# Kernel tuning notes

Hardware: AMD Instinct MI355X
Metric: run time of the kernel (lower is better)

The kernel has to match this reference:

```python
import jax, jax.numpy as jnp
import numpy as np

B, L, M = 4, 2048, 1024
G, E = 8, 8
CAP_FACTOR = 2.0

def _ffn_size(m, widening=8.0):
    f = int(widening * m) * 2 // 3
    return f + (8 - f) % 8

H = _ffn_size(M)  # 5464


def setup_inputs():
    key = jax.random.key(0)
    k0, k1, k2, k3, k4 = jax.random.split(key, 5)
    return {
        "inputs": jax.random.normal(k0, (B, L, M), jnp.float32),
        "router_w": jax.random.normal(k1, (M, E), jnp.float32) * 0.02,
        "w0_kernel": jax.random.normal(k2, (E, M, H), jnp.float32) * 0.02,
        "w1_kernel": jax.random.normal(k3, (E, M, H), jnp.float32) * 0.02,
        "wo_kernel": jax.random.normal(k4, (E, H, M), jnp.float32) * 0.02,
    }


def _gating_top2(logits, C):
    # logits: (G, S, E) -> dispatch, combine: (G, S, E, C)
    Gd, Sd, Ed = logits.shape
    raw = jax.nn.softmax(logits, axis=-1)
    idx1 = jnp.argmax(raw, axis=-1)
    m1 = jax.nn.one_hot(idx1, Ed, dtype=logits.dtype)
    gate1 = jnp.sum(raw * m1, axis=-1)
    rest = raw * (1.0 - m1)
    idx2 = jnp.argmax(rest, axis=-1)
    m2 = jax.nn.one_hot(idx2, Ed, dtype=logits.dtype)
    gate2 = jnp.sum(rest * m2, axis=-1)
    # exclusive cumsum along S gives position in expert queue
    p1 = jnp.cumsum(m1, axis=-2) - m1
    m1 = m1 * (p1 < C).astype(m1.dtype)
    p1 = jnp.sum(p1 * m1, axis=-1)
    m1_flat = jnp.sum(m1, axis=-1)
    m1_count = jnp.sum(m1, axis=-2)  # (G, E)
    p2 = jnp.cumsum(m2, axis=-2) - m2 + m1_count[:, None, :]
    m2 = m2 * (p2 < C).astype(m2.dtype)
    p2 = jnp.sum(p2 * m2, axis=-1)
    m2_flat = jnp.sum(m2, axis=-1)
    gate1 = gate1 * m1_flat
    gate2 = gate2 * m2_flat
    c1 = (gate1[..., None] * jax.nn.one_hot(idx1, Ed, dtype=jnp.float32))[..., None] \
         * jax.nn.one_hot(p1.astype(jnp.int32), C, dtype=jnp.float32)[:, :, None, :]
    c2 = (gate2[..., None] * jax.nn.one_hot(idx2, Ed, dtype=jnp.float32))[..., None] \
         * jax.nn.one_hot(p2.astype(jnp.int32), C, dtype=jnp.float32)[:, :, None, :]
    combine = (c1 + c2).astype(logits.dtype)
    dispatch = (combine != 0).astype(logits.dtype)
    return dispatch, combine


def reference(inputs, router_w, w0_kernel, w1_kernel, wo_kernel):
    Bb, Ll, Mm = inputs.shape
    S = Bb * Ll // G
    x = inputs.reshape(G, S, Mm)
    logits = jnp.einsum('GSM,ME->GSE', x, router_w)
    cap = int(CAP_FACTOR * S / E)
    C = (cap + 3) // 4 * 4
    dispatch, combine = _gating_top2(logits, C)
    expert_inputs = jnp.einsum('GSEC,GSM->EGCM', dispatch, x)
    layer_w0 = jnp.einsum('EGCM,EMH->EGCH', expert_inputs, w0_kernel)
    layer_w1 = jnp.einsum('EGCM,EMH->EGCH', expert_inputs, w1_kernel)
    hidden = jax.nn.gelu(layer_w0, approximate=True) * layer_w1
    expert_outputs = jnp.einsum('EGCH,EHM->EGCM', hidden, wo_kernel)
    out = jnp.einsum('EGCM,GSEC->GSM', expert_outputs, combine)
    return out.reshape(Bb, Ll, Mm)
```

## Files before the change

kernel.cpp:

```cpp
#include <hip/hip_runtime.h>
#include <cstdint>
#include <cstddef>

constexpr int G = 8;
constexpr int S = 1024;
constexpr int E = 8;
constexpr int MD = 1024;
constexpr int H = 5464;
constexpr int HP = 5504;
constexpr int CAP = 256;
constexpr int T = G * S;
constexpr int GC = G * CAP;

typedef __bf16 bf16;
typedef __bf16 bf16x8 __attribute__((ext_vector_type(8)));
typedef __bf16 bf16x4 __attribute__((ext_vector_type(4)));
typedef float f32x4 __attribute__((ext_vector_type(4)));

__device__ __forceinline__ void async16(const void* g, void* l) {
    __builtin_amdgcn_global_load_lds((__attribute__((address_space(1))) void*)(g),
                                     (__attribute__((address_space(3))) void*)(l),
                                     16, 0, 0);
}

__device__ __forceinline__ float gelu_tanh(float x) {
    return 0.5f * x * (1.0f + tanhf(0.7978845608028654f * (x + 0.044715f * x * x * x)));
}

__device__ __forceinline__ int sw_elem(int row, int gi) {
    return (row * 8 + (gi ^ (row & 7))) * 8;
}

__global__ void router_k(const float* __restrict__ x, const float* __restrict__ rw,
                         int* __restrict__ idx1, int* __restrict__ idx2,
                         float* __restrict__ gate1, float* __restrict__ gate2) {
    int wave = threadIdx.x >> 6, lane = threadIdx.x & 63;
    int t = blockIdx.x * 4 + wave;
    const float* xr = x + (size_t)t * MD;
    float acc[E];
#pragma unroll
    for (int e = 0; e < E; e++) acc[e] = 0.0f;
    for (int m = lane; m < MD; m += 64) {
        float xv = xr[m];
        const float* w = rw + m * E;
#pragma unroll
        for (int e = 0; e < E; e++) acc[e] += xv * w[e];
    }
#pragma unroll
    for (int off = 32; off > 0; off >>= 1) {
#pragma unroll
        for (int e = 0; e < E; e++) acc[e] += __shfl_xor(acc[e], off, 64);
    }
    if (lane == 0) {
        float mx = acc[0];
#pragma unroll
        for (int e = 1; e < E; e++) mx = fmaxf(mx, acc[e]);
        float raw[E]; float sum = 0.0f;
#pragma unroll
        for (int e = 0; e < E; e++) { raw[e] = expf(acc[e] - mx); sum += raw[e]; }
        float inv = 1.0f / sum;
#pragma unroll
        for (int e = 0; e < E; e++) raw[e] *= inv;
        int i1 = 0; float b1 = raw[0];
#pragma unroll
        for (int e = 1; e < E; e++) if (raw[e] > b1) { b1 = raw[e]; i1 = e; }
        int i2 = 0; float b2 = -1.0f;
#pragma unroll
        for (int e = 0; e < E; e++) {
            float v = (e == i1) ? 0.0f : raw[e];
            if (v > b2) { b2 = v; i2 = e; }
        }
        idx1[t] = i1; idx2[t] = i2; gate1[t] = b1; gate2[t] = b2;
    }
}

__global__ void scan_k(const int* __restrict__ idx1, const int* __restrict__ idx2,
                       const float* __restrict__ gate1, const float* __restrict__ gate2,
                       int* __restrict__ tok1, int* __restrict__ tok2,
                       float* __restrict__ g1m, float* __restrict__ g2m,
                       int* __restrict__ slot_src, int* __restrict__ fill) {
    int g = blockIdx.x;
    int lane = threadIdx.x;
    unsigned long long lt = (1ull << lane) - 1ull;
    int cnt1[E], cnt2[E];
#pragma unroll
    for (int e = 0; e < E; e++) { cnt1[e] = 0; cnt2[e] = 0; }
    for (int ch = 0; ch < S / 64; ch++) {
        int s = ch * 64 + lane, t = g * S + s;
        int i1 = idx1[t];
        int p = 0;
#pragma unroll
        for (int e = 0; e < E; e++) {
            unsigned long long m = __ballot(i1 == e);
            if (i1 == e) p = cnt1[e] + (int)__popcll(m & lt);
            cnt1[e] += (int)__popcll(m);
        }
        bool kept = p < CAP;
        tok1[t] = kept ? (i1 * CAP + p) : -1;
        g1m[t] = kept ? gate1[t] : 0.0f;
        if (kept) slot_src[((i1 * G + g) << 8) + p] = s;
    }
    int m1c[E];
#pragma unroll
    for (int e = 0; e < E; e++) m1c[e] = min(cnt1[e], CAP);
    for (int ch = 0; ch < S / 64; ch++) {
        int s = ch * 64 + lane, t = g * S + s;
        int i2 = idx2[t];
        float g2 = gate2[t];
        int p = 0;
#pragma unroll
        for (int e = 0; e < E; e++) {
            unsigned long long m = __ballot(i2 == e);
            if (i2 == e) p = m1c[e] + cnt2[e] + (int)__popcll(m & lt);
            cnt2[e] += (int)__popcll(m);
        }
        bool kept = p < CAP;
        bool nz = (g2 != 0.0f);
        tok2[t] = (kept && nz) ? (i2 * CAP + p) : -1;
        g2m[t] = (kept && nz) ? g2 : 0.0f;
        if (kept) slot_src[((i2 * G + g) << 8) + p] = nz ? s : -1;
    }
    if (lane < E) fill[lane * G + g] = min(m1c[lane] + cnt2[lane], CAP);
}

__global__ void gather_k(const float* __restrict__ x, const int* __restrict__ slot_src,
                         const int* __restrict__ fill, bf16* __restrict__ ein) {
    int slot = blockIdx.x;
    int c = slot & 255, g = (slot >> 8) & 7, e = slot >> 11;
    int i = threadIdx.x * 4;
    int src = (c < fill[e * G + g]) ? slot_src[slot] : -1;
    bf16x4 v;
    if (src >= 0) {
        float4 f = *(const float4*)(x + ((size_t)(g * S + src)) * MD + i);
        v[0] = (bf16)f.x; v[1] = (bf16)f.y; v[2] = (bf16)f.z; v[3] = (bf16)f.w;
    } else {
        v[0] = (bf16)0.0f; v[1] = (bf16)0.0f; v[2] = (bf16)0.0f; v[3] = (bf16)0.0f;
    }
    *(bf16x4*)(ein + (size_t)slot * MD + i) = v;
}

__global__ void transpose_cast_k(const float* __restrict__ in, bf16* __restrict__ out,
                                 int R, int Cc, int Rp, int Cp) {
    __shared__ float lds[64][65];
    int c0 = blockIdx.x * 64;
    int r0 = blockIdx.y * 64;
    const float* bin = in + (size_t)blockIdx.z * R * Cc;
    bf16* bout = out + (size_t)blockIdx.z * Cp * Rp;
    int tid = threadIdx.x;
    int lr = tid >> 4;
    int lc = (tid & 15) * 4;
#pragma unroll
    for (int i = 0; i < 4; i++) {
        int r = r0 + lr + i * 16;
        float v0 = 0, v1 = 0, v2 = 0, v3 = 0;
        if (r < R) {
            const float* p = bin + (size_t)r * Cc + c0 + lc;
            if (c0 + lc + 3 < Cc) {
                float4 f = *(const float4*)p;
                v0 = f.x; v1 = f.y; v2 = f.z; v3 = f.w;
            } else {
                if (c0 + lc + 0 < Cc) v0 = p[0];
                if (c0 + lc + 1 < Cc) v1 = p[1];
                if (c0 + lc + 2 < Cc) v2 = p[2];
                if (c0 + lc + 3 < Cc) v3 = p[3];
            }
        }
        lds[lr + i * 16][lc + 0] = v0;
        lds[lr + i * 16][lc + 1] = v1;
        lds[lr + i * 16][lc + 2] = v2;
        lds[lr + i * 16][lc + 3] = v3;
    }
    __syncthreads();
    int orr = tid >> 2;
    int oc = (tid & 3) * 16;
    bf16x8 o0, o1;
#pragma unroll
    for (int j = 0; j < 8; j++) o0[j] = (bf16)lds[oc + j][orr];
#pragma unroll
    for (int j = 0; j < 8; j++) o1[j] = (bf16)lds[oc + 8 + j][orr];
    bf16* dst = bout + (size_t)(c0 + orr) * Rp + r0 + oc;
    *(bf16x8*)(dst) = o0;
    *(bf16x8*)(dst + 8) = o1;
}

__global__ __launch_bounds__(256, 3) void gemm1_k(const bf16* __restrict__ ein,
                                                  const bf16* __restrict__ w0t,
                                                  const bf16* __restrict__ w1t,
                                                  bf16* __restrict__ hidden) {
    int rt = blockIdx.x, nt = blockIdx.y, e = blockIdx.z;
    __shared__ __align__(16) bf16 As[128 * 64];
    __shared__ __align__(16) bf16 B0s[64 * 64];
    __shared__ __align__(16) bf16 B1s[64 * 64];
    int lane = threadIdx.x & 63, wave = threadIdx.x >> 6;
    int wm = wave & 1, wn = wave >> 1;
    const bf16* A  = ein + ((size_t)e * GC + rt * 128) * MD;
    const bf16* B0 = w0t + ((size_t)e * HP + nt * 64) * MD;
    const bf16* B1 = w1t + ((size_t)e * HP + nt * 64) * MD;
    f32x4 acc0[4][2], acc1[4][2];
    f32x4 z = {0.0f, 0.0f, 0.0f, 0.0f};
#pragma unroll
    for (int i = 0; i < 4; i++)
#pragma unroll
        for (int j = 0; j < 2; j++) { acc0[i][j] = z; acc1[i][j] = z; }
    int lr = lane >> 3, ls = lane & 7;
#pragma unroll 1
    for (int kt = 0; kt < MD / 64; kt++) {
        __syncthreads();
        int k0 = kt * 64;
#pragma unroll
        for (int i = 0; i < 4; i++) {
            int c = i * 4 + wave;
            int r = c * 8 + lr;
            int gj = ls ^ (r & 7);
            async16(A + (size_t)r * MD + k0 + gj * 8, &As[c * 512]);
        }
#pragma unroll
        for (int i = 0; i < 2; i++) {
            int c = i * 4 + wave;
            int r = c * 8 + lr;
            int gj = ls ^ (r & 7);
            size_t go = (size_t)r * MD + k0 + gj * 8;
            async16(B0 + go, &B0s[c * 512]);
            async16(B1 + go, &B1s[c * 512]);
        }
        __syncthreads();
#pragma unroll
        for (int ks = 0; ks < 2; ks++) {
            bf16x8 af[4], b0f[2], b1f[2];
            int gi = ks * 4 + (lane >> 4);
            int mrow = wm * 64 + (lane & 15);
            int nrow = wn * 32 + (lane & 15);
#pragma unroll
            for (int i = 0; i < 4; i++) af[i] = *(const bf16x8*)&As[sw_elem(mrow + i * 16, gi)];
#pragma unroll
            for (int j = 0; j < 2; j++) {
                b0f[j] = *(const bf16x8*)&B0s[sw_elem(nrow + j * 16, gi)];
                b1f[j] = *(const bf16x8*)&B1s[sw_elem(nrow + j * 16, gi)];
            }
#pragma unroll
            for (int i = 0; i < 4; i++)
#pragma unroll
                for (int j = 0; j < 2; j++) {
                    acc0[i][j] = __builtin_amdgcn_mfma_f32_16x16x32_bf16(af[i], b0f[j], acc0[i][j], 0, 0, 0);
                    acc1[i][j] = __builtin_amdgcn_mfma_f32_16x16x32_bf16(af[i], b1f[j], acc1[i][j], 0, 0, 0);
                }
        }
    }
    bf16* Hb = hidden + (size_t)e * GC * HP;
    int colb = nt * 64 + wn * 32 + (lane & 15);
    int rowb = rt * 128 + wm * 64 + ((lane >> 4) * 4);
#pragma unroll
    for (int i = 0; i < 4; i++)
#pragma unroll
        for (int j = 0; j < 2; j++) {
            int col = colb + j * 16;
            bool ok = col < H;
#pragma unroll
            for (int r = 0; r < 4; r++) {
                int row = rowb + i * 16 + r;
                float v = ok ? gelu_tanh(acc0[i][j][r]) * acc1[i][j][r] : 0.0f;
                Hb[(size_t)row * HP + col] = (bf16)v;
            }
        }
}

__global__ __launch_bounds__(256) void gemm2_k(const bf16* __restrict__ hidden,
                                               const bf16* __restrict__ wot,
                                               float* __restrict__ eout) {
    int rt = blockIdx.x, nt = blockIdx.y, e = blockIdx.z;
    __shared__ __align__(16) bf16 As[128 * 64];
    __shared__ __align__(16) bf16 Bs[128 * 64];
    int lane = threadIdx.x & 63, wave = threadIdx.x >> 6;
    int wm = wave & 1, wn = wave >> 1;
    const bf16* A = hidden + ((size_t)e * GC + rt * 128) * HP;
    const bf16* B = wot + ((size_t)e * MD + nt * 128) * HP;
    f32x4 acc[4][4];
    f32x4 z = {0.0f, 0.0f, 0.0f, 0.0f};
#pragma unroll
    for (int i = 0; i < 4; i++)
#pragma unroll
        for (int j = 0; j < 4; j++) acc[i][j] = z;
    int lr = lane >> 3, ls = lane & 7;
#pragma unroll 1
    for (int kt = 0; kt < HP / 64; kt++) {
        __syncthreads();
        int k0 = kt * 64;
#pragma unroll
        for (int i = 0; i < 4; i++) {
            int R0 = (i * 4 + wave) * 8;
            int r = R0 + lr;
            int gj = ls ^ (r & 7);
            size_t go = (size_t)r * HP + k0 + gj * 8;
            async16(A + go, &As[R0 * 64]);
            async16(B + go, &Bs[R0 * 64]);
        }
        __syncthreads();
#pragma unroll
        for (int ks = 0; ks < 2; ks++) {
            bf16x8 af[4], bf[4];
            int gi = ks * 4 + (lane >> 4);
            int mrow = wm * 64 + (lane & 15);
            int nrow = wn * 64 + (lane & 15);
#pragma unroll
            for (int i = 0; i < 4; i++) {
                af[i] = *(const bf16x8*)&As[sw_elem(mrow + i * 16, gi)];
                bf[i] = *(const bf16x8*)&Bs[sw_elem(nrow + i * 16, gi)];
            }
#pragma unroll
            for (int i = 0; i < 4; i++)
#pragma unroll
                for (int j = 0; j < 4; j++)
                    acc[i][j] = __builtin_amdgcn_mfma_f32_16x16x32_bf16(af[i], bf[j], acc[i][j], 0, 0, 0);
        }
    }
    float* Ob = eout + (size_t)e * GC * MD;
    int colb = nt * 128 + wn * 64 + (lane & 15);
    int rowb = rt * 128 + wm * 64 + ((lane >> 4) * 4);
#pragma unroll
    for (int i = 0; i < 4; i++)
#pragma unroll
        for (int j = 0; j < 4; j++) {
            int col = colb + j * 16;
#pragma unroll
            for (int r = 0; r < 4; r++) {
                int row = rowb + i * 16 + r;
                Ob[(size_t)row * MD + col] = acc[i][j][r];
            }
        }
}

__global__ void combine_k(const float* __restrict__ eout, const int* __restrict__ tok1,
                          const int* __restrict__ tok2, const float* __restrict__ g1m,
                          const float* __restrict__ g2m, float* __restrict__ out) {
    int t = blockIdx.x;
    int g = t >> 10;
    int i = threadIdx.x * 4;
    int r1 = tok1[t], r2 = tok2[t];
    float f1 = g1m[t], f2 = g2m[t];
    float4 o = {0, 0, 0, 0};
    if (r1 >= 0) {
        size_t row = (size_t)(((r1 >> 8) * G + g) * CAP + (r1 & 255));
        float4 v = *(const float4*)(eout + row * MD + i);
        o.x += f1 * v.x; o.y += f1 * v.y; o.z += f1 * v.z; o.w += f1 * v.w;
    }
    if (r2 >= 0) {
        size_t row = (size_t)(((r2 >> 8) * G + g) * CAP + (r2 & 255));
        float4 v = *(const float4*)(eout + row * MD + i);
        o.x += f2 * v.x; o.y += f2 * v.y; o.z += f2 * v.z; o.w += f2 * v.w;
    }
    *(float4*)(out + (size_t)t * MD + i) = o;
}

constexpr size_t SZ_TI = (size_t)T * 4;
constexpr size_t OFF_IDX1 = 0;
constexpr size_t OFF_IDX2 = OFF_IDX1 + SZ_TI;
constexpr size_t OFF_GT1  = OFF_IDX2 + SZ_TI;
constexpr size_t OFF_GT2  = OFF_GT1 + SZ_TI;
constexpr size_t OFF_G1M  = OFF_GT2 + SZ_TI;
constexpr size_t OFF_G2M  = OFF_G1M + SZ_TI;
constexpr size_t OFF_TK1  = OFF_G2M + SZ_TI;
constexpr size_t OFF_TK2  = OFF_TK1 + SZ_TI;
constexpr size_t OFF_SLOT = OFF_TK2 + SZ_TI;
constexpr size_t OFF_FILL = OFF_SLOT + (size_t)E * G * CAP * 4;
constexpr size_t OFF_EIN  = (OFF_FILL + (size_t)E * G * 4 + 255) & ~(size_t)255;
constexpr size_t OFF_W0T  = OFF_EIN + (size_t)E * GC * MD * 2;
constexpr size_t OFF_W1T  = OFF_W0T + (size_t)E * HP * MD * 2;
constexpr size_t OFF_WOT  = OFF_W1T + (size_t)E * HP * MD * 2;
constexpr size_t OFF_HID  = OFF_WOT + (size_t)E * MD * HP * 2;
constexpr size_t OFF_EOUT = OFF_HID + (size_t)E * GC * HP * 2;

extern "C" void kernel_launch(void* const* d_in, const int* in_sizes, int n_in,
                              void* d_out, int out_size, void* d_ws, size_t ws_size,
                              hipStream_t stream) {
    const float* x  = (const float*)d_in[0];
    const float* rw = (const float*)d_in[1];
    const float* w0 = (const float*)d_in[2];
    const float* w1 = (const float*)d_in[3];
    const float* wo = (const float*)d_in[4];
    float* out = (float*)d_out;
    char* ws = (char*)d_ws;

    int*   idx1 = (int*)(ws + OFF_IDX1);
    int*   idx2 = (int*)(ws + OFF_IDX2);
    float* gt1  = (float*)(ws + OFF_GT1);
    float* gt2  = (float*)(ws + OFF_GT2);
    float* g1m  = (float*)(ws + OFF_G1M);
    float* g2m  = (float*)(ws + OFF_G2M);
    int*   tk1  = (int*)(ws + OFF_TK1);
    int*   tk2  = (int*)(ws + OFF_TK2);
    int*   slot = (int*)(ws + OFF_SLOT);
    int*   fill = (int*)(ws + OFF_FILL);
    bf16*  ein  = (bf16*)(ws + OFF_EIN);
    bf16*  w0t  = (bf16*)(ws + OFF_W0T);
    bf16*  w1t  = (bf16*)(ws + OFF_W1T);
    bf16*  wot  = (bf16*)(ws + OFF_WOT);
    bf16*  hid  = (bf16*)(ws + OFF_HID);
    float* eout = (float*)(ws + OFF_EOUT);

    router_k<<<T / 4, 256, 0, stream>>>(x, rw, idx1, idx2, gt1, gt2);
    scan_k<<<G, 64, 0, stream>>>(idx1, idx2, gt1, gt2, tk1, tk2, g1m, g2m, slot, fill);
    gather_k<<<E * G * CAP, 256, 0, stream>>>(x, slot, fill, ein);
    transpose_cast_k<<<dim3(HP / 64, MD / 64, E), 256, 0, stream>>>(w0, w0t, MD, H, MD, HP);
    transpose_cast_k<<<dim3(HP / 64, MD / 64, E), 256, 0, stream>>>(w1, w1t, MD, H, MD, HP);
    transpose_cast_k<<<dim3(MD / 64, HP / 64, E), 256, 0, stream>>>(wo, wot, H, MD, HP, MD);
    gemm1_k<<<dim3(GC / 128, HP / 64, E), 256, 0, stream>>>(ein, w0t, w1t, hid);
    gemm2_k<<<dim3(GC / 128, MD / 128, E), 256, 0, stream>>>(hid, wot, eout);
    combine_k<<<T, 256, 0, stream>>>(eout, tk1, tk2, g1m, g2m, out);
}
```

Before: 1.249 ms.

## Use 256x256 double-buffered 8-wave GEMM core with interleaved w0/w1 layout

Both expert GEMMs now share a 256x256 output tile core run by 512 threads. It double-buffers LDS, prefetches half-tiles between MFMA quadrants, raises wave priority during MFMA and uses explicit waitcnt/barrier control. The w0 and w1 transposes write into one interleaved buffer in 128-column blocks, so gemm1 runs as a single GEMM over width 2*HP. The GELU-times-w1 product is formed in the epilogue from paired accumulators, and block IDs are swizzled for L2 locality. This targets low arithmetic intensity and unhidden load latency, at the cost of 128KB of LDS per block and hand-written synchronization that is fragile.

After: 1.208 ms. 3.3% less time.

```diff
diff --git a/kernel.cpp b/kernel.cpp
--- a/kernel.cpp
+++ b/kernel.cpp
@@ -8,9 +8,11 @@
 constexpr int MD = 1024;
 constexpr int H = 5464;
 constexpr int HP = 5504;
+constexpr int N1 = 2 * HP;
 constexpr int CAP = 256;
 constexpr int T = G * S;
 constexpr int GC = G * CAP;
+constexpr int BK = 64;
 
 typedef __bf16 bf16;
 typedef __bf16 bf16x8 __attribute__((ext_vector_type(8)));
@@ -30,6 +32,11 @@
 __device__ __forceinline__ int sw_elem(int row, int gi) {
     return (row * 8 + (gi ^ (row & 7))) * 8;
 }
+
+#define BARRIER()   __builtin_amdgcn_s_barrier()
+#define FENCE()     asm volatile("" ::: "memory")
+#define WAITV(n)    asm volatile("s_waitcnt vmcnt(" #n ")" ::: "memory")
+#define WAITLGKM0() asm volatile("s_waitcnt lgkmcnt(0)" ::: "memory")
 
 __global__ void router_k(const float* __restrict__ x, const float* __restrict__ rw,
                          int* __restrict__ idx1, int* __restrict__ idx2,
@@ -140,7 +147,7 @@
 }
 
 __global__ void transpose_cast_k(const float* __restrict__ in, bf16* __restrict__ out,
-                                 int R, int Cc, int Rp, int Cp) {
+                                 int R, int Cc, int Rp, int Cp, int ilv) {
     __shared__ float lds[64][65];
     int c0 = blockIdx.x * 64;
     int r0 = blockIdx.y * 64;
@@ -178,155 +185,206 @@
     for (int j = 0; j < 8; j++) o0[j] = (bf16)lds[oc + j][orr];
 #pragma unroll
     for (int j = 0; j < 8; j++) o1[j] = (bf16)lds[oc + 8 + j][orr];
-    bf16* dst = bout + (size_t)(c0 + orr) * Rp + r0 + oc;
+    int cc = c0 + orr;
+    int r01 = (ilv >= 0) ? (((cc >> 7) << 8) + ilv + (cc & 127)) : cc;
+    bf16* dst = bout + (size_t)r01 * Rp + r0 + oc;
     *(bf16x8*)(dst) = o0;
     *(bf16x8*)(dst + 8) = o1;
 }
 
-__global__ __launch_bounds__(256, 3) void gemm1_k(const bf16* __restrict__ ein,
-                                                  const bf16* __restrict__ w0t,
-                                                  const bf16* __restrict__ w1t,
+__device__ __forceinline__ void stage_half(const bf16* __restrict__ base, int ld,
+                                           bf16* lds, int half, int wave, int lr, int ls) {
+#pragma unroll
+    for (int i = 0; i < 2; i++) {
+        int c = half * 16 + wave * 2 + i;
+        int r = c * 8 + lr;
+        int gj = ls ^ (r & 7);
+        async16(base + (size_t)r * ld + gj * 8, lds + c * 512);
+    }
+    FENCE();
+}
+
+template<int NT>
+__device__ __forceinline__ void mm256_core(const bf16* __restrict__ A,
+                                           const bf16* __restrict__ B,
+                                           int lda, int ldb,
+                                           bf16* sA0, bf16* sA1, bf16* sB0, bf16* sB1,
+                                           f32x4 (&acc)[8][4]) {
+    int lane = threadIdx.x & 63, wave = threadIdx.x >> 6;
+    int wm = wave >> 2, wn = wave & 3;
+    int lr = lane >> 3, ls = lane & 7;
+    int mr = lane & 15, kq = lane >> 4;
+
+    stage_half(A, lda, sA0, 0, wave, lr, ls);
+    stage_half(B, ldb, sB0, 0, wave, lr, ls);
+    stage_half(A, lda, sA0, 1, wave, lr, ls);
+    stage_half(B, ldb, sB0, 1, wave, lr, ls);
+
+    f32x4 z = {0.0f, 0.0f, 0.0f, 0.0f};
+#pragma unroll
+    for (int i = 0; i < 8; i++)
+#pragma unroll
+        for (int j = 0; j < 4; j++) acc[i][j] = z;
+
+    WAITV(4);
+    BARRIER();
+
+#pragma unroll 1
+    for (int t = 0; t < NT; ++t) {
+        bf16* Ad = (t & 1) ? sA1 : sA0;
+        bf16* Bd = (t & 1) ? sB1 : sB0;
+        bf16* An = (t & 1) ? sA0 : sA1;
+        bf16* Bn = (t & 1) ? sB0 : sB1;
+        const bf16* Ax = A + (size_t)(t + 1) * BK;
+        const bf16* Bx = B + (size_t)(t + 1) * BK;
+        bool pf = (t + 1 < NT);
+        bf16x8 a0[4][2], a1[4][2], b0[2][2], b1[2][2];
+
+#pragma unroll
+        for (int i = 0; i < 4; i++)
+#pragma unroll
+            for (int ks = 0; ks < 2; ks++)
+                a0[i][ks] = *(const bf16x8*)&Ad[sw_elem(wm * 64 + i * 16 + mr, ks * 4 + kq)];
+#pragma unroll
+        for (int j = 0; j < 2; j++)
+#pragma unroll
+            for (int ks = 0; ks < 2; ks++)
+                b0[j][ks] = *(const bf16x8*)&Bd[sw_elem(wn * 32 + j * 16 + mr, ks * 4 + kq)];
+        if (pf) { stage_half(Ax, lda, An, 0, wave, lr, ls); WAITV(2); }
+        else    { WAITV(0); }
+        BARRIER();
+        WAITLGKM0();
+        __builtin_amdgcn_s_setprio(1);
+#pragma unroll
+        for (int ks = 0; ks < 2; ks++)
+#pragma unroll
+            for (int i = 0; i < 4; i++)
+#pragma unroll
+                for (int j = 0; j < 2; j++)
+                    acc[i][j] = __builtin_amdgcn_mfma_f32_16x16x32_bf16(a0[i][ks], b0[j][ks], acc[i][j], 0, 0, 0);
+        __builtin_amdgcn_s_setprio(0);
+        BARRIER();
+
+#pragma unroll
+        for (int j = 0; j < 2; j++)
+#pragma unroll
+            for (int ks = 0; ks < 2; ks++)
+                b1[j][ks] = *(const bf16x8*)&Bd[sw_elem(128 + wn * 32 + j * 16 + mr, ks * 4 + kq)];
+        if (pf) stage_half(Bx, ldb, Bn, 0, wave, lr, ls);
+        BARRIER();
+        WAITLGKM0();
+        __builtin_amdgcn_s_setprio(1);
+#pragma unroll
+        for (int ks = 0; ks < 2; ks++)
+#pragma unroll
+            for (int i = 0; i < 4; i++)
+#pragma unroll
+                for (int j = 0; j < 2; j++)
+                    acc[i][2 + j] = __builtin_amdgcn_mfma_f32_16x16x32_bf16(a0[i][ks], b1[j][ks], acc[i][2 + j], 0, 0, 0);
+        __builtin_amdgcn_s_setprio(0);
+        BARRIER();
+
+#pragma unroll
+        for (int i = 0; i < 4; i++)
+#pragma unroll
+            for (int ks = 0; ks < 2; ks++)
+                a1[i][ks] = *(const bf16x8*)&Ad[sw_elem(128 + wm * 64 + i * 16 + mr, ks * 4 + kq)];
+        if (pf) stage_half(Ax, lda, An, 1, wave, lr, ls);
+        BARRIER();
+        WAITLGKM0();
+        __builtin_amdgcn_s_setprio(1);
+#pragma unroll
+        for (int ks = 0; ks < 2; ks++)
+#pragma unroll
+            for (int i = 0; i < 4; i++)
+#pragma unroll
+                for (int j = 0; j < 2; j++)
+                    acc[4 + i][2 + j] = __builtin_amdgcn_mfma_f32_16x16x32_bf16(a1[i][ks], b1[j][ks], acc[4 + i][2 + j], 0, 0, 0);
+        __builtin_amdgcn_s_setprio(0);
+        BARRIER();
+
+        if (pf) { stage_half(Bx, ldb, Bn, 1, wave, lr, ls); WAITV(4); }
+        else    { WAITV(0); }
+        BARRIER();
+        __builtin_amdgcn_s_setprio(1);
+#pragma unroll
+        for (int ks = 0; ks < 2; ks++)
+#pragma unroll
+            for (int i = 0; i < 4; i++)
+#pragma unroll
+                for (int j = 0; j < 2; j++)
+                    acc[4 + i][j] = __builtin_amdgcn_mfma_f32_16x16x32_bf16(a1[i][ks], b0[j][ks], acc[4 + i][j], 0, 0, 0);
+        __builtin_amdgcn_s_setprio(0);
+        BARRIER();
+    }
+}
+
+__global__ __launch_bounds__(512, 2) void gemm1_k(const bf16* __restrict__ ein,
+                                                  const bf16* __restrict__ w01t,
                                                   bf16* __restrict__ hidden) {
-    int rt = blockIdx.x, nt = blockIdx.y, e = blockIdx.z;
-    __shared__ __align__(16) bf16 As[128 * 64];
-    __shared__ __align__(16) bf16 B0s[64 * 64];
-    __shared__ __align__(16) bf16 B1s[64 * 64];
+    __shared__ __align__(16) bf16 smem[4 * 256 * BK];
+    int flat = blockIdx.x;
+    int chunk = gridDim.x >> 3;
+    int swz = (flat & 7) * chunk + (flat >> 3);
+    constexpr int NTL = N1 / 256;
+    int e = swz / (8 * NTL);
+    int rem = swz - e * (8 * NTL);
+    int rt = rem & 7;
+    int nt = rem >> 3;
+    const bf16* A = ein  + ((size_t)e * GC + (size_t)rt * 256) * MD;
+    const bf16* B = w01t + ((size_t)e * N1 + (size_t)nt * 256) * MD;
+    f32x4 acc[8][4];
+    mm256_core<MD / BK>(A, B, MD, MD, smem, smem + 16384, smem + 32768, smem + 49152, acc);
+
     int lane = threadIdx.x & 63, wave = threadIdx.x >> 6;
-    int wm = wave & 1, wn = wave >> 1;
-    const bf16* A  = ein + ((size_t)e * GC + rt * 128) * MD;
-    const bf16* B0 = w0t + ((size_t)e * HP + nt * 64) * MD;
-    const bf16* B1 = w1t + ((size_t)e * HP + nt * 64) * MD;
-    f32x4 acc0[4][2], acc1[4][2];
-    f32x4 z = {0.0f, 0.0f, 0.0f, 0.0f};
-#pragma unroll
-    for (int i = 0; i < 4; i++)
-#pragma unroll
-        for (int j = 0; j < 2; j++) { acc0[i][j] = z; acc1[i][j] = z; }
-    int lr = lane >> 3, ls = lane & 7;
-#pragma unroll 1
-    for (int kt = 0; kt < MD / 64; kt++) {
-        __syncthreads();
-        int k0 = kt * 64;
-#pragma unroll
-        for (int i = 0; i < 4; i++) {
-            int c = i * 4 + wave;
-            int r = c * 8 + lr;
-            int gj = ls ^ (r & 7);
-            async16(A + (size_t)r * MD + k0 + gj * 8, &As[c * 512]);
-        }
-#pragma unroll
-        for (int i = 0; i < 2; i++) {
-            int c = i * 4 + wave;
-            int r = c * 8 + lr;
-            int gj = ls ^ (r & 7);
-            size_t go = (size_t)r * MD + k0 + gj * 8;
-            async16(B0 + go, &B0s[c * 512]);
-            async16(B1 + go, &B1s[c * 512]);
-        }
-        __syncthreads();
-#pragma unroll
-        for (int ks = 0; ks < 2; ks++) {
-            bf16x8 af[4], b0f[2], b1f[2];
-            int gi = ks * 4 + (lane >> 4);
-            int mrow = wm * 64 + (lane & 15);
-            int nrow = wn * 32 + (lane & 15);
-#pragma unroll
-            for (int i = 0; i < 4; i++) af[i] = *(const bf16x8*)&As[sw_elem(mrow + i * 16, gi)];
-#pragma unroll
-            for (int j = 0; j < 2; j++) {
-                b0f[j] = *(const bf16x8*)&B0s[sw_elem(nrow + j * 16, gi)];
-                b1f[j] = *(const bf16x8*)&B1s[sw_elem(nrow + j * 16, gi)];
+    int wm = wave >> 2, wn = wave & 3;
+    bf16* Hb = hidden + (size_t)e * GC * HP;
+#pragma unroll
+    for (int i = 0; i < 8; i++) {
+        int rowb = rt * 256 + (i >> 2) * 128 + wm * 64 + (i & 3) * 16 + (lane >> 4) * 4;
+#pragma unroll
+        for (int j = 0; j < 2; j++) {
+            int col = nt * 128 + wn * 32 + j * 16 + (lane & 15);
+            bool ok = col < H;
+#pragma unroll
+            for (int r = 0; r < 4; r++) {
+                float v = ok ? gelu_tanh(acc[i][j][r]) * acc[i][j + 2][r] : 0.0f;
+                Hb[(size_t)(rowb + r) * HP + col] = (bf16)v;
             }
-#pragma unroll
-            for (int i = 0; i < 4; i++)
-#pragma unroll
-                for (int j = 0; j < 2; j++) {
-                    acc0[i][j] = __builtin_amdgcn_mfma_f32_16x16x32_bf16(af[i], b0f[j], acc0[i][j], 0, 0, 0);
-                    acc1[i][j] = __builtin_amdgcn_mfma_f32_16x16x32_bf16(af[i], b1f[j], acc1[i][j], 0, 0, 0);
-                }
-        }
-    }
-    bf16* Hb = hidden + (size_t)e * GC * HP;
-    int colb = nt * 64 + wn * 32 + (lane & 15);
-    int rowb = rt * 128 + wm * 64 + ((lane >> 4) * 4);
-#pragma unroll
-    for (int i = 0; i < 4; i++)
-#pragma unroll
-        for (int j = 0; j < 2; j++) {
-            int col = colb + j * 16;
-            bool ok = col < H;
-#pragma unroll
-            for (int r = 0; r < 4; r++) {
-                int row = rowb + i * 16 + r;
-                float v = ok ? gelu_tanh(acc0[i][j][r]) * acc1[i][j][r] : 0.0f;
-                Hb[(size_t)row * HP + col] = (bf16)v;
-            }
-        }
-}
-
-__global__ __launch_bounds__(256) void gemm2_k(const bf16* __restrict__ hidden,
-                                               const bf16* __restrict__ wot,
-                                               float* __restrict__ eout) {
-    int rt = blockIdx.x, nt = blockIdx.y, e = blockIdx.z;
-    __shared__ __align__(16) bf16 As[128 * 64];
-    __shared__ __align__(16) bf16 Bs[128 * 64];
+        }
+    }
+}
+
+__global__ __launch_bounds__(512, 2) void gemm2_k(const bf16* __restrict__ hidden,
+                                                  const bf16* __restrict__ wot,
+                                                  float* __restrict__ eout) {
+    __shared__ __align__(16) bf16 smem[4 * 256 * BK];
+    int flat = blockIdx.x;
+    int chunk = gridDim.x >> 3;
+    int swz = (flat & 7) * chunk + (flat >> 3);
+    int e = swz >> 5;
+    int rem = swz & 31;
+    int rt = rem & 7;
+    int nt = rem >> 3;
+    const bf16* A = hidden + ((size_t)e * GC + (size_t)rt * 256) * HP;
+    const bf16* B = wot    + ((size_t)e * MD + (size_t)nt * 256) * HP;
+    f32x4 acc[8][4];
+    mm256_core<HP / BK>(A, B, HP, HP, smem, smem + 16384, smem + 32768, smem + 49152, acc);
+
     int lane = threadIdx.x & 63, wave = threadIdx.x >> 6;
-    int wm = wave & 1, wn = wave >> 1;
-    const bf16* A = hidden + ((size_t)e * GC + rt * 128) * HP;
-    const bf16* B = wot + ((size_t)e * MD + nt * 128) * HP;
-    f32x4 acc[4][4];
-    f32x4 z = {0.0f, 0.0f, 0.0f, 0.0f};
-#pragma unroll
-    for (int i = 0; i < 4; i++)
-#pragma unroll
-        for (int j = 0; j < 4; j++) acc[i][j] = z;
-    int lr = lane >> 3, ls = lane & 7;
-#pragma unroll 1
-    for (int kt = 0; kt < HP / 64; kt++) {
-        __syncthreads();
-        int k0 = kt * 64;
-#pragma unroll
-        for (int i = 0; i < 4; i++) {
-            int R0 = (i * 4 + wave) * 8;
-            int r = R0 + lr;
-            int gj = ls ^ (r & 7);
-            size_t go = (size_t)r * HP + k0 + gj * 8;
-            async16(A + go, &As[R0 * 64]);
-            async16(B + go, &Bs[R0 * 64]);
-        }
-        __syncthreads();
-#pragma unroll
-        for (int ks = 0; ks < 2; ks++) {
-            bf16x8 af[4], bf[4];
-            int gi = ks * 4 + (lane >> 4);
-            int mrow = wm * 64 + (lane & 15);
-            int nrow = wn * 64 + (lane & 15);
-#pragma unroll
-            for (int i = 0; i < 4; i++) {
-                af[i] = *(const bf16x8*)&As[sw_elem(mrow + i * 16, gi)];
-                bf[i] = *(const bf16x8*)&Bs[sw_elem(nrow + i * 16, gi)];
-            }
-#pragma unroll
-            for (int i = 0; i < 4; i++)
-#pragma unroll
-                for (int j = 0; j < 4; j++)
-                    acc[i][j] = __builtin_amdgcn_mfma_f32_16x16x32_bf16(af[i], bf[j], acc[i][j], 0, 0, 0);
-        }
-    }
+    int wm = wave >> 2, wn = wave & 3;
     float* Ob = eout + (size_t)e * GC * MD;
-    int colb = nt * 128 + wn * 64 + (lane & 15);
-    int rowb = rt * 128 + wm * 64 + ((lane >> 4) * 4);
-#pragma unroll
-    for (int i = 0; i < 4; i++)
+#pragma unroll
+    for (int i = 0; i < 8; i++) {
+        int rowb = rt * 256 + (i >> 2) * 128 + wm * 64 + (i & 3) * 16 + (lane >> 4) * 4;
 #pragma unroll
         for (int j = 0; j < 4; j++) {
-            int col = colb + j * 16;
-#pragma unroll
-            for (int r = 0; r < 4; r++) {
-                int row = rowb + i * 16 + r;
-                Ob[(size_t)row * MD + col] = acc[i][j][r];
-            }
-        }
+            int col = nt * 256 + (j >> 1) * 128 + wn * 32 + (j & 1) * 16 + (lane & 15);
+#pragma unroll
+            for (int r = 0; r < 4; r++)
+                Ob[(size_t)(rowb + r) * MD + col] = acc[i][j][r];
+        }
+    }
 }
 
 __global__ void combine_k(const float* __restrict__ eout, const int* __restrict__ tok1,
@@ -363,9 +421,8 @@
 constexpr size_t OFF_SLOT = OFF_TK2 + SZ_TI;
 constexpr size_t OFF_FILL = OFF_SLOT + (size_t)E * G * CAP * 4;
 constexpr size_t OFF_EIN  = (OFF_FILL + (size_t)E * G * 4 + 255) & ~(size_t)255;
-constexpr size_t OFF_W0T  = OFF_EIN + (size_t)E * GC * MD * 2;
-constexpr size_t OFF_W1T  = OFF_W0T + (size_t)E * HP * MD * 2;
-constexpr size_t OFF_WOT  = OFF_W1T + (size_t)E * HP * MD * 2;
+constexpr size_t OFF_W01T = OFF_EIN + (size_t)E * GC * MD * 2;
+constexpr size_t OFF_WOT  = OFF_W01T + (size_t)E * N1 * MD * 2;
 constexpr size_t OFF_HID  = OFF_WOT + (size_t)E * MD * HP * 2;
 constexpr size_t OFF_EOUT = OFF_HID + (size_t)E * GC * HP * 2;
 
@@ -391,8 +448,7 @@
     int*   slot = (int*)(ws + OFF_SLOT);
     int*   fill = (int*)(ws + OFF_FILL);
     bf16*  ein  = (bf16*)(ws + OFF_EIN);
-    bf16*  w0t  = (bf16*)(ws + OFF_W0T);
-    bf16*  w1t  = (bf16*)(ws + OFF_W1T);
+    bf16*  w01t = (bf16*)(ws + OFF_W01T);
     bf16*  wot  = (bf16*)(ws + OFF_WOT);
     bf16*  hid  = (bf16*)(ws + OFF_HID);
     float* eout = (float*)(ws + OFF_EOUT);
@@ -400,10 +456,10 @@
     router_k<<<T / 4, 256, 0, stream>>>(x, rw, idx1, idx2, gt1, gt2);
     scan_k<<<G, 64, 0, stream>>>(idx1, idx2, gt1, gt2, tk1, tk2, g1m, g2m, slot, fill);
     gather_k<<<E * G * CAP, 256, 0, stream>>>(x, slot, fill, ein);
-    transpose_cast_k<<<dim3(HP / 64, MD / 64, E), 256, 0, stream>>>(w0, w0t, MD, H, MD, HP);
-    transpose_cast_k<<<dim3(HP / 64, MD / 64, E), 256, 0, stream>>>(w1, w1t, MD, H, MD, HP);
-    transpose_cast_k<<<dim3(MD / 64, HP / 64, E), 256, 0, stream>>>(wo, wot, H, MD, HP, MD);
-    gemm1_k<<<dim3(GC / 128, HP / 64, E), 256, 0, stream>>>(ein, w0t, w1t, hid);
-    gemm2_k<<<dim3(GC / 128, MD / 128, E), 256, 0, stream>>>(hid, wot, eout);
+    transpose_cast_k<<<dim3(HP / 64, MD / 64, E), 256, 0, stream>>>(w0, w01t, MD, H, MD, N1, 0);
+    transpose_cast_k<<<dim3(HP / 64, MD / 64, E), 256, 0, stream>>>(w1, w01t, MD, H, MD, N1, 128);
+    transpose_cast_k<<<dim3(MD / 64, HP / 64, E), 256, 0, stream>>>(wo, wot, H, MD, HP, MD, -1);
+    gemm1_k<<<dim3((GC / 256) * (N1 / 256) * E), 512, 0, stream>>>(ein, w01t, hid);
+    gemm2_k<<<dim3((GC / 256) * (MD / 256) * E), 512, 0, stream>>>(hid, wot, eout);
     combine_k<<<T, 256, 0, stream>>>(eout, tk1, tk2, g1m, g2m, out);
 }
```
